# Optimization experiments

Measured on AMD Instinct MI355X. Metric: run time of the kernel, lower is better.

The kernel has to match this reference:

```python
import jax, jax.numpy as jnp
import numpy as np

B = 4096        # num_graphs
N = 524288      # total nodes per node type
D_IN = 128
D_OUT = 256     # embedding_out_shape (hard-coded in module)


def _make_ptr(key, n, b):
    inner = jnp.sort(jax.random.randint(key, (b - 1,), 0, n + 1)).astype(jnp.int32)
    return jnp.concatenate([jnp.zeros(1, jnp.int32), inner, jnp.full((1,), n, jnp.int32)])


def setup_inputs() -> dict:
    key = jax.random.key(0)
    ks = jax.random.split(key, 8)
    s = 1.0 / np.sqrt(D_IN)
    return {
        "x_a": jax.random.normal(ks[0], (N, D_IN), jnp.float32),
        "W_a": jax.random.uniform(ks[1], (D_IN, D_OUT), jnp.float32, -s, s),
        "b_a": jax.random.uniform(ks[2], (D_OUT,), jnp.float32, -s, s),
        "x_b": jax.random.normal(ks[3], (N, D_IN), jnp.float32),
        "W_b": jax.random.uniform(ks[4], (D_IN, D_OUT), jnp.float32, -s, s),
        "b_b": jax.random.uniform(ks[5], (D_OUT,), jnp.float32, -s, s),
        "ptr_a": _make_ptr(ks[6], N, B),
        "ptr_b": _make_ptr(ks[7], N, B),
    }


def _segment_mean_from_ptr(y, ptr, num_graphs):
    # node i belongs to graph g s.t. ptr[g] <= i < ptr[g+1]
    n = y.shape[0]
    seg = jnp.searchsorted(ptr, jnp.arange(n, dtype=ptr.dtype), side='right') - 1
    sums = jax.ops.segment_sum(y, seg, num_segments=num_graphs)  # [B, D_OUT]
    counts = (ptr[1:] - ptr[:-1]).astype(y.dtype)                # [B]
    # empty graphs keep zero rows (sums are 0; divide by 1)
    return sums / jnp.maximum(counts, 1)[:, None]


def reference(x_a, W_a, b_a, x_b, W_b, b_b, ptr_a, ptr_b):
    y_a = x_a @ W_a + b_a  # set encoder for node type a
    y_b = x_b @ W_b + b_b  # set encoder for node type b
    e_a = _segment_mean_from_ptr(y_a, ptr_a, B)
    e_b = _segment_mean_from_ptr(y_b, ptr_b, B)
    return jnp.concatenate([e_a, e_b], axis=1)  # [B, 2*D_OUT]
```

## Files before the change

kernel.cpp:

```cpp
#include <hip/hip_runtime.h>
#include <stdint.h>

#define NGRAPHS 4096
#define NNODES  524288
#define DIN     128
#define DOUT    256
#define TILE    512
#define G2      8


__global__ __launch_bounds__(256)
void zero_ws(float4* __restrict__ ws) {
    ws[(size_t)blockIdx.x * 256 + threadIdx.x] = make_float4(0.f, 0.f, 0.f, 0.f);
}

__global__ __launch_bounds__(256, 8)
void seg_sum_kernel(const float* __restrict__ x_a, const int* __restrict__ ptr_a,
                    const float* __restrict__ x_b, const int* __restrict__ ptr_b,
                    float* __restrict__ sums) {
    const int t = blockIdx.y;
    const float* __restrict__ x   = t ? x_b  : x_a;
    const int*   __restrict__ ptr = t ? ptr_b : ptr_a;
    float* __restrict__ seg = sums + (size_t)t * NGRAPHS * DIN;

    const int r0 = blockIdx.x * TILE;
    const int r1 = r0 + TILE;

    const int tid  = threadIdx.x;
    const int slot = tid & 31;
    const int r    = tid >> 5;

    __shared__ float red[8][DIN];

    int lo = 0, hi = NGRAPHS;
    while (lo < hi) {
        int mid = (lo + hi) >> 1;
        if (ptr[mid] <= r0) lo = mid + 1; else hi = mid;
    }
    int g = lo - 1;

    const float* __restrict__ xs = x + (size_t)slot * 4;

    for (;;) {
        const int ss = ptr[g];
        const int ee = ptr[g + 1];
        const int a  = ss > r0 ? ss : r0;
        const int b  = ee < r1 ? ee : r1;

        if (b > a) {
            float4 acc = make_float4(0.f, 0.f, 0.f, 0.f);
            for (int i = a + r; i < b; i += 8) {
                const float4 v = *(const float4*)(xs + (size_t)i * DIN);
                acc.x += v.x; acc.y += v.y; acc.z += v.z; acc.w += v.w;
            }
            red[r][slot * 4 + 0] = acc.x;
            red[r][slot * 4 + 1] = acc.y;
            red[r][slot * 4 + 2] = acc.z;
            red[r][slot * 4 + 3] = acc.w;
            __syncthreads();
            if (tid < DIN) {
                float v = 0.f;
#pragma unroll
                for (int rr = 0; rr < 8; ++rr) v += red[rr][tid];
                float* dst = seg + (size_t)g * DIN + tid;
                if (ss >= r0 && ee <= r1) *dst = v;
                else                      atomicAdd(dst, v);
            }
            __syncthreads();
        }
        if (ee >= r1) break;
        ++g;
    }
}

__global__ __launch_bounds__(256)
void seg_mm_kernel(const float* __restrict__ W_a, const float* __restrict__ b_a,
                   const int* __restrict__ ptr_a,
                   const float* __restrict__ W_b, const float* __restrict__ b_b,
                   const int* __restrict__ ptr_b,
                   const float* __restrict__ sums, float* __restrict__ out) {
    const int t = blockIdx.y;
    const float* __restrict__ W    = t ? W_b  : W_a;
    const float* __restrict__ bias = t ? b_b  : b_a;
    const int*   __restrict__ ptr  = t ? ptr_b : ptr_a;
    const float* __restrict__ seg  = sums + (size_t)t * NGRAPHS * DIN;

    const int g0  = blockIdx.x * G2;
    const int tid = threadIdx.x;

    __shared__ __align__(16) float mean[G2][DIN];
    __shared__ float cnt[G2];

    if (tid < G2) {
        int n = ptr[g0 + tid + 1] - ptr[g0 + tid];
        cnt[tid] = (float)(n > 0 ? n : 1);
    }
    __syncthreads();
    for (int idx = tid; idx < G2 * DIN; idx += 256) {
        int gg = idx >> 7, k = idx & 127;
        mean[gg][k] = seg[(size_t)(g0 + gg) * DIN + k] / cnt[gg];
    }
    __syncthreads();

    float acc[G2];
#pragma unroll
    for (int gg = 0; gg < G2; ++gg) acc[gg] = 0.f;

    const float* __restrict__ wcol = W + tid;
    for (int k = 0; k < DIN; k += 4) {
        float w0 = wcol[(size_t)(k + 0) * DOUT];
        float w1 = wcol[(size_t)(k + 1) * DOUT];
        float w2 = wcol[(size_t)(k + 2) * DOUT];
        float w3 = wcol[(size_t)(k + 3) * DOUT];
#pragma unroll
        for (int gg = 0; gg < G2; ++gg) {
            const float4 m = *(const float4*)&mean[gg][k];
            acc[gg] += m.x * w0 + m.y * w1 + m.z * w2 + m.w * w3;
        }
    }

    const float bv = bias[tid];
#pragma unroll
    for (int gg = 0; gg < G2; ++gg) {
        const int g = g0 + gg;
        const int n = ptr[g + 1] - ptr[g];
        out[(size_t)g * (2 * DOUT) + t * DOUT + tid] = (n > 0) ? acc[gg] + bv : 0.f;
    }
}

__global__ __launch_bounds__(256)
void seg_encode_fallback(const float* __restrict__ x_a, const float* __restrict__ W_a,
                         const float* __restrict__ b_a, const int* __restrict__ ptr_a,
                         const float* __restrict__ x_b, const float* __restrict__ W_b,
                         const float* __restrict__ b_b, const int* __restrict__ ptr_b,
                         float* __restrict__ out) {
    const int g   = blockIdx.x;
    const int t   = blockIdx.y;
    const int tid = threadIdx.x;

    const float* __restrict__ x    = t ? x_b  : x_a;
    const float* __restrict__ W    = t ? W_b  : W_a;
    const float* __restrict__ bias = t ? b_b  : b_a;
    const int*   __restrict__ ptr  = t ? ptr_b : ptr_a;

    const int s = ptr[g];
    const int e = ptr[g + 1];
    const int n = e - s;

    float* __restrict__ orow = out + (size_t)g * (2 * DOUT) + t * DOUT;
    if (n == 0) { orow[tid] = 0.0f; return; }

    __shared__ float red[8][DIN];
    __shared__ float mean[DIN];

    const int slot = tid & 31;
    const int r    = tid >> 5;
    float4 acc = make_float4(0.f, 0.f, 0.f, 0.f);
    const float* __restrict__ xs = x + (size_t)slot * 4;
    for (int i = s + r; i < e; i += 8) {
        float4 v = *(const float4*)(xs + (size_t)i * DIN);
        acc.x += v.x; acc.y += v.y; acc.z += v.z; acc.w += v.w;
    }
    red[r][slot * 4 + 0] = acc.x;
    red[r][slot * 4 + 1] = acc.y;
    red[r][slot * 4 + 2] = acc.z;
    red[r][slot * 4 + 3] = acc.w;
    __syncthreads();
    if (tid < DIN) {
        float sum = 0.0f;
#pragma unroll
        for (int rr = 0; rr < 8; ++rr) sum += red[rr][tid];
        mean[tid] = sum * (1.0f / (float)n);
    }
    __syncthreads();
    float o = bias[tid];
    const float* __restrict__ wcol = W + tid;
#pragma unroll 8
    for (int k = 0; k < DIN; ++k) o += mean[k] * wcol[(size_t)k * DOUT];
    orow[tid] = o;
}

extern "C" void kernel_launch(void* const* d_in, const int* in_sizes, int n_in,
                              void* d_out, int out_size, void* d_ws, size_t ws_size,
                              hipStream_t stream) {
    const float* x_a  = (const float*)d_in[0];
    const float* W_a  = (const float*)d_in[1];
    const float* b_a  = (const float*)d_in[2];
    const float* x_b  = (const float*)d_in[3];
    const float* W_b  = (const float*)d_in[4];
    const float* b_b  = (const float*)d_in[5];
    const int*   ptr_a = (const int*)d_in[6];
    const int*   ptr_b = (const int*)d_in[7];
    float* out = (float*)d_out;

    const size_t ws_needed = (size_t)2 * NGRAPHS * DIN * sizeof(float);

    if (d_ws == nullptr || ws_size < ws_needed) {
        dim3 grid(NGRAPHS, 2);
        seg_encode_fallback<<<grid, 256, 0, stream>>>(x_a, W_a, b_a, ptr_a,
                                                      x_b, W_b, b_b, ptr_b, out);
        return;
    }

    float* sums = (float*)d_ws;

    zero_ws<<<(2 * NGRAPHS * DIN) / (256 * 4), 256, 0, stream>>>((float4*)sums);

    dim3 grid1(NNODES / TILE, 2);
    seg_sum_kernel<<<grid1, 256, 0, stream>>>(x_a, ptr_a, x_b, ptr_b, sums);

    dim3 grid2(NGRAPHS / G2, 2);
    seg_mm_kernel<<<grid2, 256, 0, stream>>>(W_a, b_a, ptr_a, W_b, b_b, ptr_b,
                                             sums, out);
}
```

Before: 545.6 us.

## Replace block-wide LDS reduction with per-wave shuffle and atomics in segment sum

Each 64-lane wave now reduces its partial sums with a cross-half shuffle and adds them straight to the workspace with atomics, so the shared-memory reduction and the two block barriers per segment are gone. Rows are interleaved across waves, and the accumulation loop is unrolled by four to keep more loads in flight. In exchange, each segment now costs up to four times as many global float atomics, one set per wave, including segments that lie wholly inside the tile, and float atomic ordering makes results nondeterministic.

Result: no change. 556.1 us (+1.9%).

```diff
diff --git a/kernel.cpp b/kernel.cpp
--- a/kernel.cpp
+++ b/kernel.cpp
@@ -27,10 +27,10 @@
     const int r1 = r0 + TILE;
 
     const int tid  = threadIdx.x;
-    const int slot = tid & 31;
-    const int r    = tid >> 5;
-
-    __shared__ float red[8][DIN];
+    const int lane = tid & 63;
+    const int w    = tid >> 6;
+    const int slot = lane & 31;
+    const int rr   = lane >> 5;
 
     int lo = 0, hi = NGRAPHS;
     while (lo < hi) {
@@ -47,26 +47,39 @@
         const int a  = ss > r0 ? ss : r0;
         const int b  = ee < r1 ? ee : r1;
 
-        if (b > a) {
+        if (b > a + 2 * w) {
             float4 acc = make_float4(0.f, 0.f, 0.f, 0.f);
-            for (int i = a + r; i < b; i += 8) {
-                const float4 v = *(const float4*)(xs + (size_t)i * DIN);
+            int i = a + 2 * w + rr;
+
+            for (; i + 24 < b; i += 32) {
+                float4 v0 = *(const float4*)(xs + (size_t)(i     ) * DIN);
+                float4 v1 = *(const float4*)(xs + (size_t)(i +  8) * DIN);
+                float4 v2 = *(const float4*)(xs + (size_t)(i + 16) * DIN);
+                float4 v3 = *(const float4*)(xs + (size_t)(i + 24) * DIN);
+                v0.x += v1.x; v0.y += v1.y; v0.z += v1.z; v0.w += v1.w;
+                v2.x += v3.x; v2.y += v3.y; v2.z += v3.z; v2.w += v3.w;
+                acc.x += v0.x + v2.x;
+                acc.y += v0.y + v2.y;
+                acc.z += v0.z + v2.z;
+                acc.w += v0.w + v2.w;
+            }
+            for (; i < b; i += 8) {
+                float4 v = *(const float4*)(xs + (size_t)i * DIN);
                 acc.x += v.x; acc.y += v.y; acc.z += v.z; acc.w += v.w;
             }
-            red[r][slot * 4 + 0] = acc.x;
-            red[r][slot * 4 + 1] = acc.y;
-            red[r][slot * 4 + 2] = acc.z;
-            red[r][slot * 4 + 3] = acc.w;
-            __syncthreads();
-            if (tid < DIN) {
-                float v = 0.f;
-#pragma unroll
-                for (int rr = 0; rr < 8; ++rr) v += red[rr][tid];
-                float* dst = seg + (size_t)g * DIN + tid;
-                if (ss >= r0 && ee <= r1) *dst = v;
-                else                      atomicAdd(dst, v);
+
+            acc.x += __shfl_xor(acc.x, 32);
+            acc.y += __shfl_xor(acc.y, 32);
+            acc.z += __shfl_xor(acc.z, 32);
+            acc.w += __shfl_xor(acc.w, 32);
+
+            if (lane < 32) {
+                float* dst = seg + (size_t)g * DIN + slot * 4;
+                atomicAdd(dst + 0, acc.x);
+                atomicAdd(dst + 1, acc.y);
+                atomicAdd(dst + 2, acc.z);
+                atomicAdd(dst + 3, acc.w);
             }
-            __syncthreads();
         }
         if (ee >= r1) break;
         ++g;
```
